# Kernel tuning notes

Hardware: AMD Instinct MI355X
Metric: run time of the kernel (lower is better)

## Reference

```python
import jax, jax.numpy as jnp
import numpy as np

MARGIN = 0.2
NEG_INF = -1e30
POS_INF = 1e30


def setup_inputs() -> dict:
    key = jax.random.key(0)
    k1, k2 = jax.random.split(key)
    B, D = 8192, 128
    im = jax.random.normal(k1, (B, D), dtype=jnp.float32)
    ids = jax.random.randint(k2, (B,), 0, 512, dtype=jnp.int64)
    return {"im": im, "ids": ids}


def reference(im, ids):
    # scores[i, j] = <im_i, im_j>, with the diagonal zeroed (as in the original,
    # which sets scores[j][j] = 0 before mining). Note the positive set includes
    # the anchor itself, so min over positives includes the zeroed diagonal.
    B = im.shape[0]
    scores = im @ im.T                      # [B, B]
    scores = scores * (1.0 - jnp.eye(B, dtype=scores.dtype))
    pos_mask = ids[:, None] == ids[None, :]  # same id (includes self)
    neg_mask = ~pos_mask
    max_neg = jnp.max(jnp.where(neg_mask, scores, NEG_INF), axis=1)  # hardest negative per anchor
    min_pos = jnp.min(jnp.where(pos_mask, scores, POS_INF), axis=1)  # hardest positive per anchor
    cost = jnp.sum(jnp.maximum(MARGIN + max_neg - min_pos, 0.0))
    return cost
```

## Files before the change

### kernel.cpp

```cpp
#include <hip/hip_runtime.h>
#include <hip/hip_bf16.h>

#define MARGIN  0.2f
#define NEG_INF -1e30f
#define POS_INF 1e30f

#define B_SZ 8192
#define D_SZ 128
#define CS   16
#define BLK_COLS 512
#define PHASE_COLS 64
#define NPH (BLK_COLS / PHASE_COLS)

typedef __bf16 bf16x8 __attribute__((ext_vector_type(8)));
typedef float  f32x4  __attribute__((ext_vector_type(4)));
typedef float  f32x16 __attribute__((ext_vector_type(16)));

__global__ __launch_bounds__(256) void k_convert(const float* __restrict__ in,
                                                 __bf16* __restrict__ out) {
    int i = (blockIdx.x * 256 + threadIdx.x) * 8;
    float4 v0 = *reinterpret_cast<const float4*>(in + i);
    float4 v1 = *reinterpret_cast<const float4*>(in + i + 4);
    bf16x8 o;
    o[0] = (__bf16)v0.x; o[1] = (__bf16)v0.y; o[2] = (__bf16)v0.z; o[3] = (__bf16)v0.w;
    o[4] = (__bf16)v1.x; o[5] = (__bf16)v1.y; o[6] = (__bf16)v1.z; o[7] = (__bf16)v1.w;
    *reinterpret_cast<bf16x8*>(out + i) = o;
}

__global__ __launch_bounds__(256, 3) void k_mine(const __bf16* __restrict__ imb,
                                                 const int* __restrict__ ids,
                                                 float* __restrict__ wsmax,
                                                 float* __restrict__ wsmin) {
    __shared__ __bf16 bpanel[2][PHASE_COLS * D_SZ];
    __shared__ int    ids_s[BLK_COLS];

    const int bid = blockIdx.x;
    const int wg  = (bid & 7) * 128 + (bid >> 3);
    const int rb  = wg & 63;
    const int cs  = wg >> 6;

    const int tid  = threadIdx.x;
    const int w    = tid >> 6;
    const int lane = tid & 63;
    const int half = lane >> 5;
    const int l5   = lane & 31;

    const int rowbase = rb * 128 + w * 32;
    const int col0    = cs * BLK_COLS;

    const int s_tile = w >> 1;
    const int s_kf0  = (w & 1) * 4;

    {
        const __bf16* src = imb + (size_t)(col0 + s_tile * 32 + l5) * D_SZ + s_kf0 * 16 + half * 8;
        #pragma unroll
        for (int j = 0; j < 4; ++j)
            __builtin_amdgcn_global_load_lds(
                (const __attribute__((address_space(1))) unsigned int*)(src + j * 16),
                (__attribute__((address_space(3))) unsigned int*)(&bpanel[0][(s_tile * 8 + s_kf0 + j) * 512]),
                16, 0, 0);
    }

    bf16x8 afrag[8];
    {
        const __bf16* p = imb + (size_t)(rowbase + l5) * D_SZ + half * 8;
        #pragma unroll
        for (int kf = 0; kf < 8; ++kf)
            afrag[kf] = *reinterpret_cast<const bf16x8*>(p + kf * 16);
    }

    int rid[16];
    #pragma unroll
    for (int r = 0; r < 16; ++r)
        rid[r] = ids[rowbase + (r & 3) + 8 * (r >> 2) + 4 * half];

    *reinterpret_cast<int2*>(&ids_s[tid * 2]) =
        *reinterpret_cast<const int2*>(ids + col0 + tid * 2);

    asm volatile("s_waitcnt vmcnt(0) lgkmcnt(0)" ::: "memory");
    __builtin_amdgcn_s_barrier();

    float mxn[16], mnp[16];
    #pragma unroll
    for (int r = 0; r < 16; ++r) { mxn[r] = NEG_INF; mnp[r] = POS_INF; }

    #pragma unroll 1
    for (int p = 0; p < NPH; ++p) {
        if (p + 1 < NPH) {
            const int nbuf = (p + 1) & 1;
            const __bf16* src = imb + (size_t)(col0 + (p + 1) * PHASE_COLS + s_tile * 32 + l5) * D_SZ
                                + s_kf0 * 16 + half * 8;
            #pragma unroll
            for (int j = 0; j < 4; ++j)
                __builtin_amdgcn_global_load_lds(
                    (const __attribute__((address_space(1))) unsigned int*)(src + j * 16),
                    (__attribute__((address_space(3))) unsigned int*)(&bpanel[nbuf][(s_tile * 8 + s_kf0 + j) * 512]),
                    16, 0, 0);
        }
        const int buf = p & 1;
        #pragma unroll
        for (int t = 0; t < 2; ++t) {
            const __bf16* bbase = &bpanel[buf][t * 4096] + (size_t)lane * 8;
            f32x16 acc = {};
            #pragma unroll
            for (int kf = 0; kf < 8; ++kf) {
                bf16x8 bfr = *reinterpret_cast<const bf16x8*>(bbase + kf * 512);
                acc = __builtin_amdgcn_mfma_f32_32x32x16_bf16(afrag[kf], bfr, acc, 0, 0, 0);
            }
            const int cid = ids_s[p * PHASE_COLS + t * 32 + l5];
            #pragma unroll
            for (int r = 0; r < 16; ++r) {
                float sv   = acc[r];
                bool  same = (rid[r] == cid);
                mxn[r] = fmaxf(mxn[r], same ? NEG_INF : sv);
                mnp[r] = fminf(mnp[r], same ? sv : POS_INF);
            }
        }
        asm volatile("s_waitcnt vmcnt(0) lgkmcnt(0)" ::: "memory");
        __builtin_amdgcn_s_barrier();
    }

    #pragma unroll
    for (int r = 0; r < 16; ++r) {
        float mx = mxn[r];
        float mn = mnp[r];
        #pragma unroll
        for (int m = 1; m < 32; m <<= 1) {
            mx = fmaxf(mx, __shfl_xor(mx, m, 64));
            mn = fminf(mn, __shfl_xor(mn, m, 64));
        }
        if (l5 == 0) {
            int row = rowbase + (r & 3) + 8 * (r >> 2) + 4 * half;
            wsmax[(size_t)row * CS + cs] = mx;
            wsmin[(size_t)row * CS + cs] = mn;
        }
    }
}

__global__ __launch_bounds__(128) void k_final(const float* __restrict__ wsmax,
                                               const float* __restrict__ wsmin,
                                               float* __restrict__ out) {
    int r = blockIdx.x * 128 + threadIdx.x;
    float mx = NEG_INF;
    float mn = 0.0f;
    #pragma unroll
    for (int c = 0; c < CS; c += 4) {
        f32x4 vx = *reinterpret_cast<const f32x4*>(wsmax + (size_t)r * CS + c);
        f32x4 vn = *reinterpret_cast<const f32x4*>(wsmin + (size_t)r * CS + c);
        mx = fmaxf(mx, fmaxf(fmaxf(vx[0], vx[1]), fmaxf(vx[2], vx[3])));
        mn = fminf(mn, fminf(fminf(vn[0], vn[1]), fminf(vn[2], vn[3])));
    }
    float cost = fmaxf(MARGIN + mx - mn, 0.0f);
    #pragma unroll
    for (int m = 1; m < 64; m <<= 1)
        cost += __shfl_xor(cost, m, 64);
    __shared__ float part[2];
    if ((threadIdx.x & 63) == 0) part[threadIdx.x >> 6] = cost;
    __syncthreads();
    if (threadIdx.x == 0)
        atomicAdd(out, part[0] + part[1]);
}

extern "C" void kernel_launch(void* const* d_in, const int* in_sizes, int n_in,
                              void* d_out, int out_size, void* d_ws, size_t ws_size,
                              hipStream_t stream) {
    const float* im  = (const float*)d_in[0];
    const int*   ids = (const int*)d_in[1];
    float*       out = (float*)d_out;

    __bf16* imb   = (__bf16*)d_ws;
    float*  wsmax = (float*)((char*)d_ws + (size_t)B_SZ * D_SZ * 2);
    float*  wsmin = wsmax + (size_t)B_SZ * CS;

    hipMemsetAsync(d_out, 0, sizeof(float), stream);

    k_convert<<<(B_SZ * D_SZ) / (256 * 8), 256, 0, stream>>>(im, imb);
    k_mine<<<64 * CS, 256, 0, stream>>>(imb, ids, wsmax, wsmin);
    k_final<<<B_SZ / 128, 128, 0, stream>>>(wsmax, wsmin, out);
}
```

Measured before the change: 98.60 us.

## Triple-buffer B panels with prefetch distance two and partial vmcnt waits

The mining kernel moves from double to triple buffering of the LDS B panel, prefetching two phases ahead and waiting with vmcnt(4) so the next phase's loads can stay in flight across the barrier. The ids LDS staging is dropped in favour of direct global loads per tile, and the final reduction kernel uses 256-thread blocks. This is meant to hide global-to-LDS latency better, at the cost of more LDS per block (which may cut occupancy) and extra global loads of column ids inside the loop, which also count toward vmcnt.

```diff
diff --git a/kernel.cpp b/kernel.cpp
--- a/kernel.cpp
+++ b/kernel.cpp
@@ -11,6 +11,7 @@
 #define BLK_COLS 512
 #define PHASE_COLS 64
 #define NPH (BLK_COLS / PHASE_COLS)
+#define NBUF 3
 
 typedef __bf16 bf16x8 __attribute__((ext_vector_type(8)));
 typedef float  f32x4  __attribute__((ext_vector_type(4)));
@@ -31,8 +32,7 @@
                                                  const int* __restrict__ ids,
                                                  float* __restrict__ wsmax,
                                                  float* __restrict__ wsmin) {
-    __shared__ __bf16 bpanel[2][PHASE_COLS * D_SZ];
-    __shared__ int    ids_s[BLK_COLS];
+    __shared__ __bf16 bpanel[NBUF][PHASE_COLS * D_SZ];
 
     const int bid = blockIdx.x;
     const int wg  = (bid & 7) * 128 + (bid >> 3);
@@ -51,16 +51,6 @@
     const int s_tile = w >> 1;
     const int s_kf0  = (w & 1) * 4;
 
-    {
-        const __bf16* src = imb + (size_t)(col0 + s_tile * 32 + l5) * D_SZ + s_kf0 * 16 + half * 8;
-        #pragma unroll
-        for (int j = 0; j < 4; ++j)
-            __builtin_amdgcn_global_load_lds(
-                (const __attribute__((address_space(1))) unsigned int*)(src + j * 16),
-                (__attribute__((address_space(3))) unsigned int*)(&bpanel[0][(s_tile * 8 + s_kf0 + j) * 512]),
-                16, 0, 0);
-    }
-
     bf16x8 afrag[8];
     {
         const __bf16* p = imb + (size_t)(rowbase + l5) * D_SZ + half * 8;
@@ -68,16 +58,23 @@
         for (int kf = 0; kf < 8; ++kf)
             afrag[kf] = *reinterpret_cast<const bf16x8*>(p + kf * 16);
     }
-
     int rid[16];
     #pragma unroll
     for (int r = 0; r < 16; ++r)
         rid[r] = ids[rowbase + (r & 3) + 8 * (r >> 2) + 4 * half];
 
-    *reinterpret_cast<int2*>(&ids_s[tid * 2]) =
-        *reinterpret_cast<const int2*>(ids + col0 + tid * 2);
-
-    asm volatile("s_waitcnt vmcnt(0) lgkmcnt(0)" ::: "memory");
+    #pragma unroll
+    for (int pp = 0; pp < 2; ++pp) {
+        const __bf16* src = imb + (size_t)(col0 + pp * PHASE_COLS + s_tile * 32 + l5) * D_SZ
+                            + s_kf0 * 16 + half * 8;
+        #pragma unroll
+        for (int j = 0; j < 4; ++j)
+            __builtin_amdgcn_global_load_lds(
+                (const __attribute__((address_space(1))) unsigned int*)(src + j * 16),
+                (__attribute__((address_space(3))) unsigned int*)(&bpanel[pp][(s_tile * 8 + s_kf0 + j) * 512]),
+                16, 0, 0);
+    }
+    asm volatile("s_waitcnt vmcnt(4)" ::: "memory");
     __builtin_amdgcn_s_barrier();
 
     float mxn[16], mnp[16];
@@ -86,18 +83,18 @@
 
     #pragma unroll 1
     for (int p = 0; p < NPH; ++p) {
-        if (p + 1 < NPH) {
-            const int nbuf = (p + 1) & 1;
-            const __bf16* src = imb + (size_t)(col0 + (p + 1) * PHASE_COLS + s_tile * 32 + l5) * D_SZ
+        if (p + 2 < NPH) {
+            const int bs = (p + 2) % NBUF;
+            const __bf16* src = imb + (size_t)(col0 + (p + 2) * PHASE_COLS + s_tile * 32 + l5) * D_SZ
                                 + s_kf0 * 16 + half * 8;
             #pragma unroll
             for (int j = 0; j < 4; ++j)
                 __builtin_amdgcn_global_load_lds(
                     (const __attribute__((address_space(1))) unsigned int*)(src + j * 16),
-                    (__attribute__((address_space(3))) unsigned int*)(&bpanel[nbuf][(s_tile * 8 + s_kf0 + j) * 512]),
+                    (__attribute__((address_space(3))) unsigned int*)(&bpanel[bs][(s_tile * 8 + s_kf0 + j) * 512]),
                     16, 0, 0);
         }
-        const int buf = p & 1;
+        const int buf = p % NBUF;
         #pragma unroll
         for (int t = 0; t < 2; ++t) {
             const __bf16* bbase = &bpanel[buf][t * 4096] + (size_t)lane * 8;
@@ -107,7 +104,7 @@
                 bf16x8 bfr = *reinterpret_cast<const bf16x8*>(bbase + kf * 512);
                 acc = __builtin_amdgcn_mfma_f32_32x32x16_bf16(afrag[kf], bfr, acc, 0, 0, 0);
             }
-            const int cid = ids_s[p * PHASE_COLS + t * 32 + l5];
+            const int cid = ids[col0 + p * PHASE_COLS + t * 32 + l5];
             #pragma unroll
             for (int r = 0; r < 16; ++r) {
                 float sv   = acc[r];
@@ -116,7 +113,11 @@
                 mnp[r] = fminf(mnp[r], same ? sv : POS_INF);
             }
         }
-        asm volatile("s_waitcnt vmcnt(0) lgkmcnt(0)" ::: "memory");
+        if (p + 2 < NPH) {
+            asm volatile("s_waitcnt vmcnt(4)" ::: "memory");
+        } else {
+            asm volatile("s_waitcnt vmcnt(0)" ::: "memory");
+        }
         __builtin_amdgcn_s_barrier();
     }
 
@@ -137,10 +138,10 @@
     }
 }
 
-__global__ __launch_bounds__(128) void k_final(const float* __restrict__ wsmax,
+__global__ __launch_bounds__(256) void k_final(const float* __restrict__ wsmax,
                                                const float* __restrict__ wsmin,
                                                float* __restrict__ out) {
-    int r = blockIdx.x * 128 + threadIdx.x;
+    int r = blockIdx.x * 256 + threadIdx.x;
     float mx = NEG_INF;
     float mn = 0.0f;
     #pragma unroll
@@ -154,11 +155,11 @@
     #pragma unroll
     for (int m = 1; m < 64; m <<= 1)
         cost += __shfl_xor(cost, m, 64);
-    __shared__ float part[2];
+    __shared__ float part[4];
     if ((threadIdx.x & 63) == 0) part[threadIdx.x >> 6] = cost;
     __syncthreads();
     if (threadIdx.x == 0)
-        atomicAdd(out, part[0] + part[1]);
+        atomicAdd(out, part[0] + part[1] + part[2] + part[3]);
 }
 
 extern "C" void kernel_launch(void* const* d_in, const int* in_sizes, int n_in,
@@ -176,5 +177,5 @@
 
     k_convert<<<(B_SZ * D_SZ) / (256 * 8), 256, 0, stream>>>(im, imb);
     k_mine<<<64 * CS, 256, 0, stream>>>(imb, ids, wsmax, wsmin);
-    k_final<<<B_SZ / 128, 128, 0, stream>>>(wsmax, wsmin, out);
+    k_final<<<B_SZ / 256, 256, 0, stream>>>(wsmax, wsmin, out);
 }
```

Measured after the change: 98.65 us. Within noise of the previous version (+0.0%).
